# Performance work log

Measured on AMD Instinct MI355X. Metric: run time of the kernel, lower is better.

The kernel has to match this reference:

```python
import jax, jax.numpy as jnp
import numpy as np
from jax import lax

EPS = 1e-5
DN = ('NCHW', 'OIHW', 'NCHW')


def _bn(x, gamma, beta, mean, var):
    # eval-mode BatchNorm2d over channel dim (axis=1)
    s = gamma / jnp.sqrt(var + EPS)
    return x * s[None, :, None, None] + (beta - mean * s)[None, :, None, None]


def setup_inputs() -> dict:
    key = jax.random.key(0)
    ks = jax.random.split(key, 12)
    B, Cin, C, H, W, NC = 128, 2048, 512, 14, 14, 200
    return {
        'feature': jax.random.normal(ks[0], (B, Cin, H, W), jnp.float32),
        'w_reduce': jax.random.normal(ks[1], (C, Cin, 1, 1), jnp.float32) * 0.02,
        'b_reduce': jax.random.normal(ks[2], (C,), jnp.float32) * 0.02,
        'bn1_gamma': jnp.ones((C,), jnp.float32),
        'bn1_beta': jnp.zeros((C,), jnp.float32),
        'bn1_mean': jax.random.normal(ks[3], (C,), jnp.float32) * 0.02,
        'bn1_var': jax.random.uniform(ks[4], (C,), jnp.float32),
        'w3': jax.random.normal(ks[5], (C, C, 3, 3), jnp.float32) * 0.02,
        'b3': jax.random.normal(ks[6], (C,), jnp.float32) * 0.02,
        'bn2_gamma': jnp.ones((C,), jnp.float32),
        'bn2_beta': jnp.zeros((C,), jnp.float32),
        'bn2_mean': jax.random.normal(ks[7], (C,), jnp.float32) * 0.02,
        'bn2_var': jax.random.uniform(ks[8], (C,), jnp.float32),
        'fc1_w': jax.random.normal(ks[9], (NC, C), jnp.float32) * 0.02,
        'fc1_b': jnp.zeros((NC,), jnp.float32),
        'fc2_w': jax.random.normal(ks[10], (NC, NC), jnp.float32) * 0.02,
        'fc2_b': jnp.zeros((NC,), jnp.float32),
    }


def reference(feature, w_reduce, b_reduce, bn1_gamma, bn1_beta, bn1_mean, bn1_var,
              w3, b3, bn2_gamma, bn2_beta, bn2_mean, bn2_var,
              fc1_w, fc1_b, fc2_w, fc2_b):
    B, _, H, W = feature.shape
    C = w_reduce.shape[0]  # 512
    # reduce: 1x1 conv + BN + ReLU
    f = lax.conv_general_dilated(feature, w_reduce, (1, 1), 'VALID', dimension_numbers=DN)
    f = f + b_reduce[None, :, None, None]
    f = jax.nn.relu(_bn(f, bn1_gamma, bn1_beta, bn1_mean, bn1_var))
    x = f.reshape(B, C, H * W)  # [B, 512, 196]
    # channel affinity + softmax(-xxt) over last dim (= the per-row loop)
    xxt = jnp.einsum('bcn,bdn->bcd', x, x)  # [B, 512, 512]
    a = jax.nn.softmax(-xxt, axis=2)
    y = jnp.einsum('bcd,bdn->bcn', a, x).reshape(B, C, H, W)
    # conv3: 3x3 conv + BN + ReLU + global avg pool
    z = lax.conv_general_dilated(y, w3, (1, 1), 'SAME', dimension_numbers=DN)
    z = z + b3[None, :, None, None]
    z = jax.nn.relu(_bn(z, bn2_gamma, bn2_beta, bn2_mean, bn2_var))
    z = jnp.mean(z, axis=(2, 3))  # [B, 512]
    # fc_channel: Linear -> ReLU -> Linear
    h = jax.nn.relu(z @ fc1_w.T + fc1_b)
    sf = h @ fc2_w.T + fc2_b
    return sf
```

## Files before the change

### kernel.cpp

```cpp
#include <hip/hip_runtime.h>

typedef __attribute__((ext_vector_type(8))) short bf16x8;
typedef __attribute__((ext_vector_type(4))) float f32x4;
typedef __attribute__((ext_vector_type(4))) short short4v;

__device__ __forceinline__ unsigned short f2bf(float x){
  unsigned u = __float_as_uint(x);
  return (unsigned short)((u + 0x7FFFu + ((u>>16)&1u)) >> 16);
}
__device__ __forceinline__ float bf2f(unsigned short b){
  return __uint_as_float(((unsigned)b)<<16);
}

typedef const __attribute__((address_space(1))) void* gas_t;
typedef __attribute__((address_space(3))) void* las_t;
__device__ __forceinline__ void gl16(const void* g, void* l){
  __builtin_amdgcn_global_load_lds((gas_t)g, (las_t)l, 16, 0, 0);
}

static constexpr size_t O_FHI  = 0;
static constexpr size_t O_FLO  = 102760448;
static constexpr size_t O_XHI  = 205520896;
static constexpr size_t O_XLO  = 239075328;
static constexpr size_t O_XT   = 272629760;
static constexpr size_t O_AMAT = 301989888;
static constexpr size_t O_WH   = 369098752;
static constexpr size_t O_WL   = 371195904;
static constexpr size_t O_W3B  = 373293056;
static constexpr size_t O_PAR  = 378011648;
static constexpr size_t O_FC1T = 378019840;
static constexpr size_t O_FC2T = 378429440;
static constexpr size_t O_ZBAR = 378589440;

__global__ void k_params(const float* br, const float* g1, const float* be1, const float* m1, const float* v1,
                         const float* b3, const float* g2, const float* be2, const float* m2, const float* v2,
                         float* par){
  int c = blockIdx.x*256 + threadIdx.x;
  if (c >= 512) return;
  float s1 = g1[c] * rsqrtf(v1[c] + 1e-5f);
  par[c] = s1;
  par[512+c] = (br[c]-m1[c])*s1 + be1[c];
  float s2 = g2[c] * rsqrtf(v2[c] + 1e-5f);
  par[1024+c] = s2;
  par[1536+c] = (b3[c]-m2[c])*s2 + be2[c];
}

__global__ void k_wrhl(const float* wr, unsigned short* wh, unsigned short* wl){
  int k = blockIdx.x*256 + threadIdx.x;
  int c = blockIdx.y;
  float v = wr[(size_t)c*2048 + k];
  unsigned short h = f2bf(v);
  wh[(size_t)c*2048 + k] = h;
  wl[(size_t)c*2048 + k] = f2bf(v - bf2f(h));
}

__global__ void k_w3c(const float* w3, unsigned short* w3c){
  int k = blockIdx.x*256 + threadIdx.x;
  int co = blockIdx.y;
  int ci0b = k/576; int r2 = k - ci0b*576;
  int tap = r2>>6;  int cio = r2&63;
  w3c[(((size_t)ci0b*9 + tap)*512 + co)*64 + cio] =
      f2bf(w3[((size_t)co*512 + ci0b*64 + cio)*9 + tap]);
}

__global__ void k_fc1t(const float* w, float* wt){
  int i = blockIdx.x*256 + threadIdx.x;
  int k = i/200, j = i - k*200;
  wt[i] = w[j*512 + k];
}
__global__ void k_fc2t(const float* w, float* wt){
  int i = blockIdx.x*256 + threadIdx.x;
  if (i >= 200*200) return;
  int k = i/200, j = i - k*200;
  wt[i] = w[j*200 + k];
}

__global__ __launch_bounds__(256) void k_zeropad(unsigned short* xhi, unsigned short* xlo){
  int rr = blockIdx.x*256 + threadIdx.x;
  float4 z = {0.f,0.f,0.f,0.f};
  float4* a = (float4*)(xhi + (size_t)rr*256 + 192);
  float4* b = (float4*)(xlo + (size_t)rr*256 + 192);
  #pragma unroll
  for (int j=0;j<8;++j){ a[j] = z; b[j] = z; }
}

__global__ __launch_bounds__(256) void k_zeroyb(unsigned short* ypad){
  int tile = blockIdx.x;
  int r = threadIdx.x;
  if (r >= 256) return;
  int hi = r>>4, lo = r&15;
  bool pad = (hi==0)||(hi==15)||(lo==0)||(lo==15);
  if (!pad) return;
  float4 z = {0.f,0.f,0.f,0.f};
  float4* p = (float4*)(ypad + ((size_t)tile*256 + r)*64);
  #pragma unroll
  for (int j=0;j<8;++j) p[j] = z;
}

__global__ __launch_bounds__(256) void k_featT(const float* __restrict__ feat,
        unsigned short* __restrict__ fhi, unsigned short* __restrict__ flo){
  __shared__ float tile[64][33];
  int b = blockIdx.z;
  int ci0 = blockIdx.y*64, p0 = blockIdx.x*32;
  int t = threadIdx.x;
  int j = t & 31, i0 = t >> 5;
  for (int rep=0; rep<8; ++rep){
    int i = rep*8 + i0;
    int p = p0 + j;
    tile[i][j] = (p<196) ? feat[((size_t)b*2048 + ci0 + i)*196 + p] : 0.f;
  }
  __syncthreads();
  int ii = t & 63, jj0 = t >> 6;
  for (int rep=0; rep<8; ++rep){
    int jj = rep*4 + jj0;
    int p = p0 + jj;
    if (p < 196){
      float v = tile[ii][jj];
      unsigned short h = f2bf(v);
      size_t o = ((size_t)b*196 + p)*2048 + ci0 + ii;
      fhi[o] = h;
      flo[o] = f2bf(v - bf2f(h));
    }
  }
}

__global__ __launch_bounds__(256) void k_conv1(
    const unsigned short* __restrict__ fhi, const unsigned short* __restrict__ flo,
    const unsigned short* __restrict__ wh,  const unsigned short* __restrict__ wl,
    const float* __restrict__ par,
    unsigned short* __restrict__ xhi, unsigned short* __restrict__ xlo,
    unsigned short* __restrict__ xT){
  __shared__ char lds[32768];
  char* Als = lds; char* Bls = lds + 16384;
  int lin = blockIdx.x;
  int sz  = (lin&7)*98 + (lin>>3);
  int mt = sz&3;
  int gt = sz>>2;
  int c0 = mt*128;
  size_t g0 = (size_t)gt*128;
  int t = threadIdx.x, lane = t&63, wid = t>>6, wm = wid&1, wn = wid>>1;
  int fq = lane>>4, fr = lane&15;
  f32x4 acc[4][4] = {};
  for (int it=0; it<96; ++it){
    int seg = it>>5, kk0 = (it&31)*64;
    const unsigned short* As = (seg<2) ? wh : wl;
    const unsigned short* Bs = (seg==1) ? flo : fhi;
    __syncthreads();
    #pragma unroll
    for (int r=0;r<4;++r){
      int L = r*256 + t;
      int row = L>>3, cs = ((L&7)^(row&7))*8;
      gl16(As + (size_t)(c0+row)*2048 + kk0 + cs, Als + L*16);
      gl16(Bs + (g0+row)*2048 + kk0 + cs, Bls + L*16);
    }
    __syncthreads();
    #pragma unroll
    for (int ks=0; ks<2; ++ks){
      int kb = ks*64 + fq*16;
      bf16x8 af[4];
      #pragma unroll
      for (int m=0;m<4;++m){
        int row = wm*64 + m*16 + fr;
        af[m] = *(const bf16x8*)(Als + row*128 + (kb ^ ((row&7)<<4)));
      }
      #pragma unroll
      for (int n=0;n<4;++n){
        int row = wn*64 + n*16 + fr;
        bf16x8 bff = *(const bf16x8*)(Bls + row*128 + (kb ^ ((row&7)<<4)));
        #pragma unroll
        for (int m=0;m<4;++m)
          acc[m][n] = __builtin_amdgcn_mfma_f32_16x16x32_bf16(af[m], bff, acc[m][n],0,0,0);
      }
    }
  }
  const float* s1 = par; const float* t1 = par+512;
  for (int m=0;m<4;++m){
    int cb = c0 + wm*64 + m*16 + fq*4;
    float sc[4], sh[4];
    for (int j=0;j<4;++j){ sc[j]=s1[cb+j]; sh[j]=t1[cb+j]; }
    for (int n=0;n<4;++n){
      int gg = (int)g0 + wn*64 + n*16 + fr;
      int b = gg/196, p = gg - b*196;
      unsigned short hs[4];
      for (int j=0;j<4;++j){
        float v = fmaxf(acc[m][n][j]*sc[j]+sh[j], 0.f);
        unsigned short h = f2bf(v);
        hs[j] = h;
        size_t ic = (size_t)b*512 + cb + j;
        xhi[ic*256 + p] = h;
        xlo[ic*256 + p] = f2bf(v - bf2f(h));
      }
      *(short4v*)(xT + ((size_t)b*224 + p)*512 + cb) = *(short4v*)hs;
    }
  }
}

__global__ __launch_bounds__(256) void k_xxt(const unsigned short* __restrict__ xhi,
        const unsigned short* __restrict__ xlo, float* __restrict__ xxt){
  __shared__ char lds[32768];
  char* Als = lds; char* Bls = lds + 16384;
  int lin = blockIdx.x;
  int sz  = (lin&7)*160 + (lin>>3);
  int b = sz/10, sub = sz - b*10;
  unsigned mtp = (3u<<18)|(2u<<16)|(2u<<14)|(1u<<12)|(1u<<10)|(1u<<8)|(0u<<6)|(0u<<4)|(0u<<2)|0u;
  unsigned ntp = (3u<<18)|(3u<<16)|(2u<<14)|(3u<<12)|(2u<<10)|(1u<<8)|(3u<<6)|(2u<<4)|(1u<<2)|0u;
  int mt = (mtp>>(2*sub))&3, nt = (ntp>>(2*sub))&3;
  int c0 = mt*128, d0 = nt*128;
  int t = threadIdx.x, lane = t&63, wid = t>>6, wm = wid&1, wn = wid>>1;
  int fq = lane>>4, fr = lane&15;
  f32x4 acc[4][4] = {};
  for (int it=0; it<12; ++it){
    int seg = it>>2, kk0 = (it&3)*64;
    const unsigned short* As = (seg<2) ? xhi : xlo;
    const unsigned short* Bs = (seg==1) ? xlo : xhi;
    __syncthreads();
    #pragma unroll
    for (int r=0;r<4;++r){
      int L = r*256 + t;
      int row = L>>3, cs = ((L&7)^(row&7))*8;
      gl16(As + ((size_t)b*512 + c0 + row)*256 + kk0 + cs, Als + L*16);
      gl16(Bs + ((size_t)b*512 + d0 + row)*256 + kk0 + cs, Bls + L*16);
    }
    __syncthreads();
    #pragma unroll
    for (int ks=0; ks<2; ++ks){
      int kb = ks*64 + fq*16;
      bf16x8 af[4];
      #pragma unroll
      for (int m=0;m<4;++m){
        int row = wm*64 + m*16 + fr;
        af[m] = *(const bf16x8*)(Als + row*128 + (kb ^ ((row&7)<<4)));
      }
      #pragma unroll
      for (int n=0;n<4;++n){
        int row = wn*64 + n*16 + fr;
        bf16x8 bff = *(const bf16x8*)(Bls + row*128 + (kb ^ ((row&7)<<4)));
        #pragma unroll
        for (int m=0;m<4;++m)
          acc[m][n] = __builtin_amdgcn_mfma_f32_16x16x32_bf16(af[m], bff, acc[m][n],0,0,0);
      }
    }
  }
  for (int m=0;m<4;++m){
    int cb = c0 + wm*64 + m*16 + fq*4;
    for (int n=0;n<4;++n){
      int d = d0 + wn*64 + n*16 + fr;
      *(float4*)(xxt + ((size_t)b*512 + d)*512 + cb) = *(float4*)&acc[m][n];
    }
  }
  if (mt != nt){
    for (int m=0;m<4;++m){
      int cb = c0 + wm*64 + m*16 + fq*4;
      for (int n=0;n<4;++n){
        int d = d0 + wn*64 + n*16 + fr;
        for (int jj=0;jj<4;++jj)
          xxt[((size_t)b*512 + cb + jj)*512 + d] = acc[m][n][jj];
      }
    }
  }
}

__global__ __launch_bounds__(256) void k_softmax(const float* __restrict__ xxt, unsigned short* __restrict__ amat){
  int row = blockIdx.x*4 + (threadIdx.x>>6);
  int lane = threadIdx.x & 63;
  const float* src = xxt + (size_t)row*512 + lane*8;
  float4 v0 = *(const float4*)src;
  float4 v1 = *(const float4*)(src+4);
  float mn = fminf(fminf(fminf(v0.x,v0.y),fminf(v0.z,v0.w)),
                   fminf(fminf(v1.x,v1.y),fminf(v1.z,v1.w)));
  for (int m=32; m; m>>=1) mn = fminf(mn, __shfl_xor(mn, m, 64));
  float e[8];
  e[0]=__expf(mn-v0.x); e[1]=__expf(mn-v0.y); e[2]=__expf(mn-v0.z); e[3]=__expf(mn-v0.w);
  e[4]=__expf(mn-v1.x); e[5]=__expf(mn-v1.y); e[6]=__expf(mn-v1.z); e[7]=__expf(mn-v1.w);
  float s = e[0]+e[1]+e[2]+e[3]+e[4]+e[5]+e[6]+e[7];
  for (int m=32; m; m>>=1) s += __shfl_xor(s, m, 64);
  float inv = 1.f/s;
  short4v p0, p1;
  for (int q=0;q<4;++q) p0[q] = (short)f2bf(e[q]*inv);
  for (int q=0;q<4;++q) p1[q] = (short)f2bf(e[4+q]*inv);
  unsigned short* dst = amat + (size_t)row*512 + lane*8;
  *(short4v*)dst = p0;
  *(short4v*)(dst+4) = p1;
}

__global__ __launch_bounds__(256) void k_pv(const unsigned short* __restrict__ amat,
        const unsigned short* __restrict__ xT, unsigned short* __restrict__ ypad){
  __shared__ char lds[30720];
  char* Als = lds; char* Bls = lds + 16384;
  int lin = blockIdx.x, per = gridDim.x>>3;
  int sz  = (lin&7)*per + (lin>>3);
  int b = sz>>3, sub = sz&7, mt = sub>>1, nt = sub&1;
  int c0 = mt*128, n0 = nt*112;
  int t = threadIdx.x, lane = t&63, wid = t>>6;
  int fq = lane>>4, fr = lane&15;
  f32x4 acc[2][7] = {};
  for (int it=0; it<8; ++it){
    int k0 = it*64;
    __syncthreads();
    #pragma unroll
    for (int r=0;r<4;++r){
      int L = r*256 + t;
      int row = L>>3, cs = ((L&7)^(row&7))*8;
      gl16(amat + ((size_t)b*512 + c0 + row)*512 + k0 + cs, Als + L*16);
    }
    #pragma unroll
    for (int r=0;r<4;++r){
      int L = r*256 + t;
      if (L < 896){
        int row = L>>3, cs = ((L&7)^(row&7))*8;
        gl16(xT + ((size_t)b*224 + n0 + row)*512 + k0 + cs, Bls + L*16);
      }
    }
    __syncthreads();
    #pragma unroll
    for (int ks=0; ks<2; ++ks){
      int kb = ks*64 + fq*16;
      bf16x8 af[2];
      #pragma unroll
      for (int m=0;m<2;++m){
        int row = wid*32 + m*16 + fr;
        af[m] = *(const bf16x8*)(Als + row*128 + (kb ^ ((row&7)<<4)));
      }
      #pragma unroll
      for (int n=0;n<7;++n){
        int row = n*16 + fr;
        bf16x8 bff = *(const bf16x8*)(Bls + row*128 + (kb ^ ((row&7)<<4)));
        #pragma unroll
        for (int m=0;m<2;++m)
          acc[m][n] = __builtin_amdgcn_mfma_f32_16x16x32_bf16(af[m], bff, acc[m][n],0,0,0);
      }
    }
  }
  for (int m=0;m<2;++m){
    int cb = c0 + wid*32 + m*16 + fq*4;
    int ci0b = cb>>6, cio = cb&63;
    for (int n=0;n<7;++n){
      int p = n0 + n*16 + fr;
      if (p < 196){
        int hh = p/14, wwp = p - hh*14;
        int prow = (hh+1)*16 + (wwp+1);
        short4v pk;
        for (int j=0;j<4;++j) pk[j] = (short)f2bf(acc[m][n][j]);
        *(short4v*)(ypad + (((size_t)b*8 + ci0b)*256 + prow)*64 + cio) = pk;
      }
    }
  }
}

__global__ __launch_bounds__(512, 4) void k_conv3(const unsigned short* __restrict__ ypad,
        const unsigned short* __restrict__ w3c, const float* __restrict__ par,
        float* __restrict__ zbar){
  __shared__ char lds[65536];
  char* WIN = lds;
  char* AB0 = lds + 32768;
  char* AB1 = lds + 49152;
  int bx = blockIdx.x;
  int xcd = bx&7, jj2 = bx>>3;
  int b = xcd*16 + (jj2>>2), cot = jj2&3;
  int c0 = cot*128;
  int t = threadIdx.x, lane = t&63, w = t>>6;
  int wm = w>>1, wn = w&1;
  int fq = lane>>4, fr = lane&15;
  int frB = (fr<14) ? fr : 13;
  bool pok = (fr<14);
  f32x4 acc[2][7] = {};
  for (int ci0=0; ci0<8; ++ci0){
    const unsigned short* wsrc = ypad + ((size_t)(b*8 + ci0)*256)*64;
    #pragma unroll
    for (int r=0;r<4;++r){
      int L = r*512 + t;
      int row = L>>3, cs = ((L&7)^(row&7))*8;
      gl16(wsrc + row*64 + cs, WIN + L*16);
    }
    {
      const unsigned short* asrc = w3c + ((size_t)(ci0*9 + 0)*512 + c0)*64;
      #pragma unroll
      for (int r=0;r<2;++r){
        int L = r*512 + t;
        int row = L>>3, cs = ((L&7)^(row&7))*8;
        gl16(asrc + row*64 + cs, AB0 + L*16);
      }
    }
    __syncthreads();
    for (int tap=0; tap<9; ++tap){
      char* Acur = (tap&1) ? AB1 : AB0;
      char* Anxt = (tap&1) ? AB0 : AB1;
      if (tap < 8){
        const unsigned short* asrc = w3c + ((size_t)(ci0*9 + tap+1)*512 + c0)*64;
        #pragma unroll
        for (int r=0;r<2;++r){
          int L = r*512 + t;
          int row = L>>3, cs = ((L&7)^(row&7))*8;
          gl16(asrc + row*64 + cs, Anxt + L*16);
        }
      }
      int kh = tap/3, kw = tap - kh*3;
      bf16x8 ah[2][2];
      #pragma unroll
      for (int ks=0;ks<2;++ks)
        #pragma unroll
        for (int m=0;m<2;++m){
          int row = wm*32 + m*16 + fr;
          ah[ks][m] = *(const bf16x8*)(Acur + row*128 + (((ks*4+fq)^(row&7))<<4));
        }
      int col = frB + kw;
      __builtin_amdgcn_s_setprio(1);
      #pragma unroll
      for (int n=0;n<7;++n){
        int prow = (wn*7 + n + kh)*16 + col;
        #pragma unroll
        for (int ks=0;ks<2;++ks){
          bf16x8 bf = *(const bf16x8*)(WIN + prow*128 + (((ks*4+fq)^(prow&7))<<4));
          acc[0][n] = __builtin_amdgcn_mfma_f32_16x16x32_bf16(ah[ks][0], bf, acc[0][n],0,0,0);
          acc[1][n] = __builtin_amdgcn_mfma_f32_16x16x32_bf16(ah[ks][1], bf, acc[1][n],0,0,0);
        }
      }
      __builtin_amdgcn_s_setprio(0);
      __syncthreads();
    }
  }
  const float* s2 = par+1024; const float* t2 = par+1536;
  float ps[2][4];
  #pragma unroll
  for (int m=0;m<2;++m){
    int cb = c0 + wm*32 + m*16 + fq*4;
    #pragma unroll
    for (int j=0;j<4;++j){
      float sc = s2[cb+j], sh = t2[cb+j];
      float s = 0.f;
      #pragma unroll
      for (int n=0;n<7;++n)
        s += fmaxf(acc[m][n][j]*sc + sh, 0.f);
      ps[m][j] = pok ? s : 0.f;
    }
  }
  #pragma unroll
  for (int off=1; off<16; off<<=1)
    #pragma unroll
    for (int m=0;m<2;++m)
      #pragma unroll
      for (int j=0;j<4;++j)
        ps[m][j] += __shfl_xor(ps[m][j], off, 64);
  float* part = (float*)lds;
  if (fr == 0){
    #pragma unroll
    for (int m=0;m<2;++m)
      #pragma unroll
      for (int j=0;j<4;++j)
        part[wn*128 + wm*32 + m*16 + fq*4 + j] = ps[m][j];
  }
  __syncthreads();
  if (t < 128)
    zbar[(size_t)b*512 + c0 + t] = part[t] + part[128 + t];
}

__global__ __launch_bounds__(256) void k_fc(const float* __restrict__ zbar,
        const float* __restrict__ fc1T, const float* __restrict__ fc1b,
        const float* __restrict__ fc2T, const float* __restrict__ fc2b,
        float* __restrict__ out){
  __shared__ float zb[512];
  __shared__ float hl[200];
  int b = blockIdx.x, t = threadIdx.x;
  zb[t]     = zbar[(size_t)b*512 + t]       * (1.f/196.f);
  zb[t+256] = zbar[(size_t)b*512 + t + 256] * (1.f/196.f);
  __syncthreads();
  if (t < 200){
    float acc = fc1b[t];
    for (int k=0;k<512;++k) acc += zb[k]*fc1T[k*200+t];
    hl[t] = fmaxf(acc, 0.f);
  }
  __syncthreads();
  if (t < 200){
    float acc = fc2b[t];
    for (int k=0;k<200;++k) acc += hl[k]*fc2T[k*200+t];
    out[(size_t)b*200 + t] = acc;
  }
}

extern "C" void kernel_launch(void* const* d_in, const int* in_sizes, int n_in,
                              void* d_out, int out_size, void* d_ws, size_t ws_size,
                              hipStream_t stream) {
  const float* feature  = (const float*)d_in[0];
  const float* w_reduce = (const float*)d_in[1];
  const float* b_reduce = (const float*)d_in[2];
  const float* g1  = (const float*)d_in[3];
  const float* be1 = (const float*)d_in[4];
  const float* m1  = (const float*)d_in[5];
  const float* v1  = (const float*)d_in[6];
  const float* w3  = (const float*)d_in[7];
  const float* b3  = (const float*)d_in[8];
  const float* g2  = (const float*)d_in[9];
  const float* be2 = (const float*)d_in[10];
  const float* m2  = (const float*)d_in[11];
  const float* v2  = (const float*)d_in[12];
  const float* fc1w = (const float*)d_in[13];
  const float* fc1b = (const float*)d_in[14];
  const float* fc2w = (const float*)d_in[15];
  const float* fc2b = (const float*)d_in[16];

  char* ws = (char*)d_ws;
  unsigned short* fhi  = (unsigned short*)(ws + O_FHI);
  unsigned short* flo  = (unsigned short*)(ws + O_FLO);
  float*          xxt  = (float*)(ws + O_FHI);
  unsigned short* xhi  = (unsigned short*)(ws + O_XHI);
  unsigned short* xlo  = (unsigned short*)(ws + O_XLO);
  unsigned short* ypad = (unsigned short*)(ws + O_XLO);
  unsigned short* xT   = (unsigned short*)(ws + O_XT);
  unsigned short* amat = (unsigned short*)(ws + O_AMAT);
  unsigned short* wh   = (unsigned short*)(ws + O_WH);
  unsigned short* wl   = (unsigned short*)(ws + O_WL);
  unsigned short* w3c  = (unsigned short*)(ws + O_W3B);
  float* par  = (float*)(ws + O_PAR);
  float* fc1T = (float*)(ws + O_FC1T);
  float* fc2T = (float*)(ws + O_FC2T);
  float* zbar = (float*)(ws + O_ZBAR);

  k_params<<<2, 256, 0, stream>>>(b_reduce, g1, be1, m1, v1, b3, g2, be2, m2, v2, par);
  k_wrhl<<<dim3(8,512), 256, 0, stream>>>(w_reduce, wh, wl);
  k_w3c<<<dim3(18,512), 256, 0, stream>>>(w3, w3c);
  k_fc1t<<<400, 256, 0, stream>>>(fc1w, fc1T);
  k_fc2t<<<157, 256, 0, stream>>>(fc2w, fc2T);
  k_zeropad<<<256, 256, 0, stream>>>(xhi, xlo);

  k_featT<<<dim3(7,32,128), 256, 0, stream>>>(feature, fhi, flo);
  k_conv1<<<784, 256, 0, stream>>>(fhi, flo, wh, wl, par, xhi, xlo, xT);

  k_xxt<<<1280, 256, 0, stream>>>(xhi, xlo, xxt);
  k_softmax<<<16384, 256, 0, stream>>>(xxt, amat);

  k_zeroyb<<<1024, 256, 0, stream>>>(ypad);
  k_pv<<<1024, 256, 0, stream>>>(amat, xT, ypad);
  k_conv3<<<512, 512, 0, stream>>>(ypad, w3c, par, zbar);
  k_fc<<<128, 256, 0, stream>>>(zbar, fc1T, fc1b, fc2T, fc2b, (float*)d_out);
}
```

Before: 686.1 us.

## Double-buffer conv1 LDS staging and share each K-chunk across hi/lo segments

The conv1 GEMM main loop now double-buffers its LDS tiles. It prefetches the next K-chunk with global_load_lds while MFMAs run on the current one, using a single waitcnt+barrier per iteration instead of two syncthreads. Each stage now loads all four operands (wh, wl, fhi, flo) for a 32-wide K slice, so the three split-bf16 products run per chunk instead of in three sequential passes over K. The swizzle is adapted to 64-byte rows. This doubles LDS use to 64KB, which may cut occupancy, and adds s_setprio hints.

```diff
diff --git a/kernel.cpp b/kernel.cpp
--- a/kernel.cpp
+++ b/kernel.cpp
@@ -130,8 +130,9 @@
     const float* __restrict__ par,
     unsigned short* __restrict__ xhi, unsigned short* __restrict__ xlo,
     unsigned short* __restrict__ xT){
-  __shared__ char lds[32768];
-  char* Als = lds; char* Bls = lds + 16384;
+  __shared__ char lds[65536];
+  char* BUF0 = lds;
+  char* BUF1 = lds + 32768;
   int lin = blockIdx.x;
   int sz  = (lin&7)*98 + (lin>>3);
   int mt = sz&3;
@@ -141,38 +142,60 @@
   int t = threadIdx.x, lane = t&63, wid = t>>6, wm = wid&1, wn = wid>>1;
   int fq = lane>>4, fr = lane&15;
   f32x4 acc[4][4] = {};
-  for (int it=0; it<96; ++it){
-    int seg = it>>5, kk0 = (it&31)*64;
-    const unsigned short* As = (seg<2) ? wh : wl;
-    const unsigned short* Bs = (seg==1) ? flo : fhi;
-    __syncthreads();
-    #pragma unroll
-    for (int r=0;r<4;++r){
-      int L = r*256 + t;
-      int row = L>>3, cs = ((L&7)^(row&7))*8;
-      gl16(As + (size_t)(c0+row)*2048 + kk0 + cs, Als + L*16);
-      gl16(Bs + (g0+row)*2048 + kk0 + cs, Bls + L*16);
-    }
-    __syncthreads();
-    #pragma unroll
-    for (int ks=0; ks<2; ++ks){
-      int kb = ks*64 + fq*16;
-      bf16x8 af[4];
+
+  auto STAGE = [&](int hc, char* buf){
+    #pragma unroll
+    for (int j=0;j<8;++j){
+      int arr = j>>1;
+      int L2 = t + ((j&1)<<8);
+      int row = L2>>2;
+      int cs = ((L2&3) ^ ((row>>1)&3))*8;
+      const unsigned short* src;
+      if (arr==0)      src = wh  + (size_t)(c0+row)*2048 + hc*32 + cs;
+      else if (arr==1) src = wl  + (size_t)(c0+row)*2048 + hc*32 + cs;
+      else if (arr==2) src = fhi + (g0+row)*2048 + hc*32 + cs;
+      else             src = flo + (g0+row)*2048 + hc*32 + cs;
+      gl16(src, buf + arr*8192 + L2*16);
+    }
+  };
+
+  STAGE(0, BUF0);
+  asm volatile("s_waitcnt vmcnt(0)" ::: "memory");
+  __builtin_amdgcn_s_barrier();
+  __builtin_amdgcn_sched_barrier(0);
+
+  for (int it=0; it<64; ++it){
+    char* cur = (it&1) ? BUF1 : BUF0;
+    char* nxt = (it&1) ? BUF0 : BUF1;
+    if (it < 63) STAGE(it+1, nxt);
+    __builtin_amdgcn_s_setprio(1);
+    #pragma unroll
+    for (int seg=0; seg<3; ++seg){
+      const char* Ab = cur + ((seg==2) ? 8192 : 0);
+      const char* Bb = cur + ((seg==1) ? 24576 : 16384);
+      bf16x8 af[4], bfr[4];
       #pragma unroll
       for (int m=0;m<4;++m){
         int row = wm*64 + m*16 + fr;
-        af[m] = *(const bf16x8*)(Als + row*128 + (kb ^ ((row&7)<<4)));
+        af[m] = *(const bf16x8*)(Ab + row*64 + ((fq*16) ^ (((row>>1)&3)<<4)));
       }
       #pragma unroll
       for (int n=0;n<4;++n){
         int row = wn*64 + n*16 + fr;
-        bf16x8 bff = *(const bf16x8*)(Bls + row*128 + (kb ^ ((row&7)<<4)));
+        bfr[n] = *(const bf16x8*)(Bb + row*64 + ((fq*16) ^ (((row>>1)&3)<<4)));
+      }
+      #pragma unroll
+      for (int n=0;n<4;++n)
         #pragma unroll
         for (int m=0;m<4;++m)
-          acc[m][n] = __builtin_amdgcn_mfma_f32_16x16x32_bf16(af[m], bff, acc[m][n],0,0,0);
-      }
-    }
-  }
+          acc[m][n] = __builtin_amdgcn_mfma_f32_16x16x32_bf16(af[m], bfr[n], acc[m][n],0,0,0);
+    }
+    __builtin_amdgcn_s_setprio(0);
+    asm volatile("s_waitcnt vmcnt(0)" ::: "memory");
+    __builtin_amdgcn_s_barrier();
+    __builtin_amdgcn_sched_barrier(0);
+  }
+
   const float* s1 = par; const float* t1 = par+512;
   for (int m=0;m<4;++m){
     int cb = c0 + wm*64 + m*16 + fq*4;
```

Result: faster. 598.8 us (-12.7%).
